# Performance work log

Measured on AMD Instinct MI355X. Metric: run time of the kernel, lower is better.

## Reference

```python
import jax, jax.numpy as jnp
import numpy as np


def setup_inputs() -> dict:
    key = jax.random.key(0)
    ks = jax.random.split(key, 8)
    B, N, D, E, S = 8, 4096, 1024, 64, 2
    H = D
    T = E * S  # total slots = 128
    return {
        "x": jax.random.normal(ks[0], (B, N, D), jnp.float32),
        "phi_w": jax.random.normal(ks[1], (T, D), jnp.float32) * 0.02,
        "fc1_w": jax.random.normal(ks[2], (E, H, D), jnp.float32) * 0.02,
        "fc1_b": jax.random.normal(ks[3], (E, H), jnp.float32) * 0.02,
        "fc2_w": jax.random.normal(ks[4], (E, D, H), jnp.float32) * 0.02,
        "fc2_b": jax.random.normal(ks[5], (E, D), jnp.float32) * 0.02,
        "out_w": jax.random.normal(ks[6], (D, D), jnp.float32) * 0.02,
        "out_b": jax.random.normal(ks[7], (D,), jnp.float32) * 0.02,
    }


def reference(x, phi_w, fc1_w, fc1_b, fc2_w, fc2_b, out_w, out_b):
    B, N, D = x.shape
    E, H, _ = fc1_w.shape
    T = phi_w.shape[0]
    S = T // E
    # dispatch logits: (B, N, T)
    logits = jnp.einsum('bnd,td->bnt', x, phi_w)
    dispatch_w = jax.nn.softmax(logits, axis=1)  # softmax over tokens
    combine_w = jax.nn.softmax(logits, axis=2)   # softmax over slots
    # dispatch: compress tokens -> slots, (B, T, D) -> (B, E, S, D)
    slots = jnp.einsum('bnt,bnd->btd', dispatch_w, x).reshape(B, E, S, D)
    # per-expert tiny MLP (no weight duplication over B)
    h = jnp.einsum('besd,ehd->besh', slots, fc1_w) + fc1_b[None, :, None, :]
    h = jax.nn.gelu(h, approximate=True)  # tanh approximation, matches torch
    out = jnp.einsum('besh,edh->besd', h, fc2_w) + fc2_b[None, :, None, :]
    out = out.reshape(B, T, D)
    # combine: expand slots -> tokens
    combined = jnp.einsum('bnt,btd->bnd', combine_w, out)
    output = jnp.einsum('bnd,od->bno', combined, out_w) + out_b
    aux_loss = jnp.asarray(0.0, dtype=x.dtype)
    return output, aux_loss
```

## Files before the change

### kernel.cpp

```cpp
#include <hip/hip_runtime.h>
#include <math.h>

#define B_ 8
#define N_ 4096
#define D_ 1024
#define E_ 64
#define T_ 128

using bf16   = __bf16;
using bf16x4 = __attribute__((ext_vector_type(4))) __bf16;
using bf16x8 = __attribute__((ext_vector_type(8))) __bf16;
using f32x4  = __attribute__((ext_vector_type(4))) float;

#define MFMA16(a, b, c) __builtin_amdgcn_mfma_f32_16x16x32_bf16(a, b, c, 0, 0, 0)
#define LDK 72

__device__ __forceinline__ bf16x8 ldsfrag(const bf16* p) {
  const int lane = threadIdx.x & 63;
  return *(const bf16x8*)(p + (lane & 15) * LDK + (lane >> 4) * 8);
}

__global__ void k_convert(const float* __restrict__ phi, const float* __restrict__ ow,
                          bf16* __restrict__ phi_bf, bf16* __restrict__ ow_bf)
{
  if (blockIdx.x < 128) {
    int i = blockIdx.x * 256 + threadIdx.x;
    float4 v = ((const float4*)phi)[i];
    ((bf16x4*)phi_bf)[i] = (bf16x4){(bf16)v.x, (bf16)v.y, (bf16)v.z, (bf16)v.w};
  } else {
    int i = (blockIdx.x - 128) * 256 + threadIdx.x;
    float4 v = ((const float4*)ow)[i];
    ((bf16x4*)ow_bf)[i] = (bf16x4){(bf16)v.x, (bf16)v.y, (bf16)v.z, (bf16)v.w};
  }
}

__global__ __launch_bounds__(256) void k_logits(
    const float* __restrict__ X, const bf16* __restrict__ Phi,
    float* __restrict__ L, bf16* __restrict__ Xbf)
{
  __shared__ bf16 As[64][LDK];
  __shared__ bf16 Bs[128][LDK];
  const int m0 = blockIdx.x * 64;
  const int tid = threadIdx.x;
  const int wave = tid >> 6, lane = tid & 63;
  const int wm = (wave >> 1) * 32;
  const int wn = (wave & 1) * 64;

  f32x4 acc[2][4];
#pragma unroll
  for (int i = 0; i < 2; ++i)
#pragma unroll
    for (int j = 0; j < 4; ++j) acc[i][j] = (f32x4){0.f, 0.f, 0.f, 0.f};

  const int ar = tid >> 2, ac = (tid & 3) * 16;
  const int br = tid >> 1, bc = (tid & 1) * 32;

  for (int k0 = 0; k0 < 1024; k0 += 64) {
    const float* xp = X + (long)(m0 + ar) * 1024 + k0 + ac;
    float4 v0 = *(const float4*)(xp + 0);
    float4 v1 = *(const float4*)(xp + 4);
    float4 v2 = *(const float4*)(xp + 8);
    float4 v3 = *(const float4*)(xp + 12);
    bf16x8 p0 = {(bf16)v0.x, (bf16)v0.y, (bf16)v0.z, (bf16)v0.w,
                 (bf16)v1.x, (bf16)v1.y, (bf16)v1.z, (bf16)v1.w};
    bf16x8 p1 = {(bf16)v2.x, (bf16)v2.y, (bf16)v2.z, (bf16)v2.w,
                 (bf16)v3.x, (bf16)v3.y, (bf16)v3.z, (bf16)v3.w};
    *(bf16x8*)&As[ar][ac]     = p0;
    *(bf16x8*)&As[ar][ac + 8] = p1;
    bf16* xo = Xbf + (long)(m0 + ar) * 1024 + k0 + ac;
    *(bf16x8*)xo       = p0;
    *(bf16x8*)(xo + 8) = p1;

    const bf16* pp = Phi + (long)br * 1024 + k0 + bc;
    *(bf16x8*)&Bs[br][bc + 0]  = *(const bf16x8*)(pp + 0);
    *(bf16x8*)&Bs[br][bc + 8]  = *(const bf16x8*)(pp + 8);
    *(bf16x8*)&Bs[br][bc + 16] = *(const bf16x8*)(pp + 16);
    *(bf16x8*)&Bs[br][bc + 24] = *(const bf16x8*)(pp + 24);
    __syncthreads();
#pragma unroll
    for (int kk = 0; kk < 64; kk += 32) {
      bf16x8 a0 = ldsfrag(&As[wm][kk]);
      bf16x8 a1 = ldsfrag(&As[wm + 16][kk]);
#pragma unroll
      for (int n = 0; n < 4; ++n) {
        bf16x8 bb = ldsfrag(&Bs[wn + n * 16][kk]);
        acc[0][n] = MFMA16(a0, bb, acc[0][n]);
        acc[1][n] = MFMA16(a1, bb, acc[1][n]);
      }
    }
    __syncthreads();
  }
  const int cc = lane & 15, rr = (lane >> 4) * 4;
#pragma unroll
  for (int m = 0; m < 2; ++m)
#pragma unroll
    for (int n = 0; n < 4; ++n)
#pragma unroll
      for (int j = 0; j < 4; ++j)
        L[(long)(m0 + wm + m * 16 + rr + j) * 128 + wn + n * 16 + cc] = acc[m][n][j];
}

__global__ __launch_bounds__(256) void disp_partial(const float* __restrict__ L,
    float* __restrict__ redM, float* __restrict__ redS)
{
  const int chunk = blockIdx.x;
  const int b     = blockIdx.y;
  const int t    = threadIdx.x & 127;
  const int half = threadIdx.x >> 7;
  const float* Lb = L + (long)b * N_ * T_;
  float m = -1e30f, s = 0.f;
  for (int i = 0; i < 64; ++i) {
    int n = chunk * 128 + i * 2 + half;
    float v = Lb[(long)n * T_ + t];
    if (v > m) { s = s * expf(m - v) + 1.f; m = v; }
    else       { s += expf(v - m); }
  }
  __shared__ float sm[128], ss[128];
  if (half) { sm[t] = m; ss[t] = s; }
  __syncthreads();
  if (!half) {
    float m2 = sm[t], s2 = ss[t];
    float nm = fmaxf(m, m2);
    float ns = s * expf(m - nm) + s2 * expf(m2 - nm);
    redM[((long)b * 32 + chunk) * 128 + t] = nm;
    redS[((long)b * 32 + chunk) * 128 + t] = ns;
  }
}

__global__ void disp_final(const float* __restrict__ redM, const float* __restrict__ redS,
                           float* __restrict__ Mf, float* __restrict__ Zf)
{
  int idx = blockIdx.x * 256 + threadIdx.x;
  int b = idx >> 7, t = idx & 127;
  float m = -1e30f, s = 0.f;
  for (int c = 0; c < 32; ++c) {
    float mc = redM[((long)b * 32 + c) * 128 + t];
    float sc = redS[((long)b * 32 + c) * 128 + t];
    float nm = fmaxf(m, mc);
    s = s * expf(m - nm) + sc * expf(mc - nm);
    m = nm;
  }
  Mf[idx] = m;
  Zf[idx] = 1.f / s;
}

__global__ __launch_bounds__(256) void k_dwt(const float* __restrict__ L,
    const float* __restrict__ Mf, const float* __restrict__ Zf, bf16* __restrict__ DWT)
{
  __shared__ float S[64][132];
  const int b = blockIdx.y, n0 = blockIdx.x * 64;
  const int tid = threadIdx.x;
  const int r = tid >> 2;
  const int c0 = (tid & 3) * 32;
  const float* Lp = L + ((long)b * N_ + n0 + r) * T_ + c0;
#pragma unroll
  for (int i = 0; i < 32; i += 4) {
    float4 v = *(const float4*)(Lp + i);
    int tb = b * 128 + c0 + i;
    S[r][c0 + i + 0] = expf(v.x - Mf[tb + 0]) * Zf[tb + 0];
    S[r][c0 + i + 1] = expf(v.y - Mf[tb + 1]) * Zf[tb + 1];
    S[r][c0 + i + 2] = expf(v.z - Mf[tb + 2]) * Zf[tb + 2];
    S[r][c0 + i + 3] = expf(v.w - Mf[tb + 3]) * Zf[tb + 3];
  }
  __syncthreads();
  const int nc = (tid & 7) * 8;
  for (int ti = tid >> 3; ti < 128; ti += 32) {
    bf16x8 o;
#pragma unroll
    for (int j = 0; j < 8; ++j) o[j] = (bf16)S[nc + j][ti];
    *(bf16x8*)(DWT + ((long)b * 128 + ti) * 4096 + n0 + nc) = o;
  }
}

__global__ __launch_bounds__(256) void k_cw(const float* __restrict__ L, bf16* __restrict__ CW)
{
  const int row  = blockIdx.x * 4 + (threadIdx.x >> 6);
  const int lane = threadIdx.x & 63;
  const float* Lr = L + (long)row * T_;
  float v0 = Lr[lane], v1 = Lr[lane + 64];
  float m = fmaxf(v0, v1);
#pragma unroll
  for (int o = 32; o; o >>= 1) m = fmaxf(m, __shfl_xor(m, o));
  float e0 = expf(v0 - m), e1 = expf(v1 - m);
  float s = e0 + e1;
#pragma unroll
  for (int o = 32; o; o >>= 1) s += __shfl_xor(s, o);
  float inv = 1.f / s;
  CW[(long)row * T_ + lane]      = (bf16)(e0 * inv);
  CW[(long)row * T_ + lane + 64] = (bf16)(e1 * inv);
}

__global__ __launch_bounds__(256) void k_slots(
    const bf16* __restrict__ DWT, const bf16* __restrict__ Xbf, float* __restrict__ Part)
{
  __shared__ bf16 As[128][LDK];
  __shared__ bf16 Bs[128][LDK];
  const int b = blockIdx.z >> 3, chunk = blockIdx.z & 7;
  const int d0 = blockIdx.x * 128;
  const int tid = threadIdx.x, wave = tid >> 6, lane = tid & 63;
  const int wm = (wave >> 1) * 64, wn = (wave & 1) * 64;

  f32x4 acc[4][4];
#pragma unroll
  for (int i = 0; i < 4; ++i)
#pragma unroll
    for (int j = 0; j < 4; ++j) acc[i][j] = (f32x4){0.f, 0.f, 0.f, 0.f};

  const int at = tid >> 1, anc = (tid & 1) * 32;
  const int bn = tid >> 2, bdc = (tid & 3) * 32;
  const long dwt_b = (long)b * 128 * 4096;
  const long x_b   = (long)b * 4096 * 1024;

  for (int k0 = 0; k0 < 512; k0 += 64) {
    const int nbase = chunk * 512 + k0;
    const bf16* ap = DWT + dwt_b + (long)at * 4096 + nbase + anc;
    *(bf16x8*)&As[at][anc + 0]  = *(const bf16x8*)(ap + 0);
    *(bf16x8*)&As[at][anc + 8]  = *(const bf16x8*)(ap + 8);
    *(bf16x8*)&As[at][anc + 16] = *(const bf16x8*)(ap + 16);
    *(bf16x8*)&As[at][anc + 24] = *(const bf16x8*)(ap + 24);
    const bf16* xp = Xbf + x_b + (long)(nbase + bn) * 1024 + d0 + bdc;
    bf16x8 q0 = *(const bf16x8*)(xp + 0);
    bf16x8 q1 = *(const bf16x8*)(xp + 8);
    bf16x8 q2 = *(const bf16x8*)(xp + 16);
    bf16x8 q3 = *(const bf16x8*)(xp + 24);
#pragma unroll
    for (int i = 0; i < 8; ++i) {
      Bs[bdc + i][bn]      = q0[i];
      Bs[bdc + 8 + i][bn]  = q1[i];
      Bs[bdc + 16 + i][bn] = q2[i];
      Bs[bdc + 24 + i][bn] = q3[i];
    }
    __syncthreads();
#pragma unroll
    for (int kk = 0; kk < 64; kk += 32) {
      bf16x8 af[4], bfr[4];
#pragma unroll
      for (int m = 0; m < 4; ++m) af[m]  = ldsfrag(&As[wm + m * 16][kk]);
#pragma unroll
      for (int n = 0; n < 4; ++n) bfr[n] = ldsfrag(&Bs[wn + n * 16][kk]);
#pragma unroll
      for (int m = 0; m < 4; ++m)
#pragma unroll
        for (int n = 0; n < 4; ++n)
          acc[m][n] = MFMA16(af[m], bfr[n], acc[m][n]);
    }
    __syncthreads();
  }
  const int cc = lane & 15, rr = (lane >> 4) * 4;
  float* Cp = Part + (long)(chunk * 8 + b) * 128 * 1024;
#pragma unroll
  for (int m = 0; m < 4; ++m)
#pragma unroll
    for (int n = 0; n < 4; ++n)
#pragma unroll
      for (int j = 0; j < 4; ++j)
        Cp[(long)(wm + m * 16 + rr + j) * 1024 + d0 + wn + n * 16 + cc] = acc[m][n][j];
}

__global__ void k_reduce8(const float* __restrict__ P, bf16* __restrict__ O)
{
  long base = ((long)blockIdx.x * 256 + threadIdx.x) * 4;
  float4 s = *(const float4*)(P + base);
  for (int c = 1; c < 8; ++c) {
    float4 v = *(const float4*)(P + (long)c * 1048576 + base);
    s.x += v.x; s.y += v.y; s.z += v.z; s.w += v.w;
  }
  *(bf16x4*)(O + base) = (bf16x4){(bf16)s.x, (bf16)s.y, (bf16)s.z, (bf16)s.w};
}

template<int GELU, int INL>
__global__ __launch_bounds__(256) void k_expert(
    const bf16* __restrict__ Ab, const float* __restrict__ W,
    const float* __restrict__ bias, bf16* __restrict__ Out)
{
  __shared__ bf16 As[16][LDK];
  __shared__ bf16 Bs[64][LDK];
  const int e = blockIdx.y;
  const int h0 = blockIdx.x * 64;
  const int tid = threadIdx.x, wave = tid >> 6, lane = tid & 63;
  f32x4 acc = (f32x4){0.f, 0.f, 0.f, 0.f};

  const int hr = tid >> 2, kc = (tid & 3) * 16;

  for (int k0 = 0; k0 < 1024; k0 += 64) {
    if (tid < 128) {
      int r = tid >> 3, akc = (tid & 7) * 8;
      long row = (INL == 0) ? (long)((r >> 1) * 128 + e * 2 + (r & 1)) : (long)(e * 16 + r);
      *(bf16x8*)&As[r][akc] = *(const bf16x8*)(Ab + row * 1024 + k0 + akc);
    }
    const float* wp = W + ((long)e * 1024 + h0 + hr) * 1024 + k0 + kc;
    float4 w0 = *(const float4*)(wp + 0);
    float4 w1 = *(const float4*)(wp + 4);
    float4 w2 = *(const float4*)(wp + 8);
    float4 w3 = *(const float4*)(wp + 12);
    bf16x8 p0 = {(bf16)w0.x, (bf16)w0.y, (bf16)w0.z, (bf16)w0.w,
                 (bf16)w1.x, (bf16)w1.y, (bf16)w1.z, (bf16)w1.w};
    bf16x8 p1 = {(bf16)w2.x, (bf16)w2.y, (bf16)w2.z, (bf16)w2.w,
                 (bf16)w3.x, (bf16)w3.y, (bf16)w3.z, (bf16)w3.w};
    *(bf16x8*)&Bs[hr][kc]     = p0;
    *(bf16x8*)&Bs[hr][kc + 8] = p1;
    __syncthreads();
#pragma unroll
    for (int kk = 0; kk < 64; kk += 32) {
      bf16x8 a  = ldsfrag(&As[0][kk]);
      bf16x8 bb = ldsfrag(&Bs[wave * 16][kk]);
      acc = MFMA16(a, bb, acc);
    }
    __syncthreads();
  }
  const int cc = lane & 15, rr = (lane >> 4) * 4;
  const int h = h0 + wave * 16 + cc;
  const float bs = bias[e * 1024 + h];
#pragma unroll
  for (int j = 0; j < 4; ++j) {
    float v = acc[j] + bs;
    if (GELU) {
      float x3 = v * v * v;
      v = 0.5f * v * (1.f + tanhf(0.7978845608028654f * (v + 0.044715f * x3)));
    }
    int m = rr + j;
    long orow = (INL == 0) ? (long)(e * 16 + m) : (long)((m >> 1) * 128 + e * 2 + (m & 1));
    Out[orow * 1024 + h] = (bf16)v;
  }
}

__global__ __launch_bounds__(256) void k_proj(
    const bf16* __restrict__ OWbf, const bf16* __restrict__ OS, bf16* __restrict__ PT)
{
  __shared__ bf16 As[64][LDK];
  __shared__ bf16 Bs[64][LDK];
  const int o0 = blockIdx.y * 64, t0 = blockIdx.x * 64;
  const int tid = threadIdx.x, wave = tid >> 6, lane = tid & 63;
  const int wm = (wave >> 1) * 32, wn = (wave & 1) * 32;
  f32x4 acc[2][2];
#pragma unroll
  for (int i = 0; i < 2; ++i)
#pragma unroll
    for (int j = 0; j < 2; ++j) acc[i][j] = (f32x4){0.f, 0.f, 0.f, 0.f};

  const int r = tid >> 2, kc = (tid & 3) * 16;
  for (int k0 = 0; k0 < 1024; k0 += 64) {
    const bf16* apo = OWbf + (long)(o0 + r) * 1024 + k0 + kc;
    *(bf16x8*)&As[r][kc]     = *(const bf16x8*)(apo + 0);
    *(bf16x8*)&As[r][kc + 8] = *(const bf16x8*)(apo + 8);
    const bf16* bpo = OS + (long)(t0 + r) * 1024 + k0 + kc;
    *(bf16x8*)&Bs[r][kc]     = *(const bf16x8*)(bpo + 0);
    *(bf16x8*)&Bs[r][kc + 8] = *(const bf16x8*)(bpo + 8);
    __syncthreads();
#pragma unroll
    for (int kk = 0; kk < 64; kk += 32) {
      bf16x8 a0 = ldsfrag(&As[wm][kk]);
      bf16x8 a1 = ldsfrag(&As[wm + 16][kk]);
      bf16x8 b0 = ldsfrag(&Bs[wn][kk]);
      bf16x8 b1 = ldsfrag(&Bs[wn + 16][kk]);
      acc[0][0] = MFMA16(a0, b0, acc[0][0]);
      acc[0][1] = MFMA16(a0, b1, acc[0][1]);
      acc[1][0] = MFMA16(a1, b0, acc[1][0]);
      acc[1][1] = MFMA16(a1, b1, acc[1][1]);
    }
    __syncthreads();
  }
  const int cc = lane & 15, rr = (lane >> 4) * 4;
#pragma unroll
  for (int m = 0; m < 2; ++m)
#pragma unroll
    for (int n = 0; n < 2; ++n)
#pragma unroll
      for (int j = 0; j < 4; ++j)
        PT[(long)(o0 + wm + m * 16 + rr + j) * 1024 + t0 + wn + n * 16 + cc] =
            (bf16)acc[m][n][j];
}

__global__ __launch_bounds__(256) void k_combine(
    const bf16* __restrict__ CW, const bf16* __restrict__ PT,
    const float* __restrict__ ob, float* __restrict__ O)
{
  __shared__ bf16 As[128][LDK];
  __shared__ bf16 Bs[128][LDK];
  const int b = blockIdx.z, m0 = blockIdx.y * 128, o0 = blockIdx.x * 128;
  const int tid = threadIdx.x, wave = tid >> 6, lane = tid & 63;
  const int wm = (wave >> 1) * 64, wn = (wave & 1) * 64;

  f32x4 acc[4][4];
#pragma unroll
  for (int i = 0; i < 4; ++i)
#pragma unroll
    for (int j = 0; j < 4; ++j) acc[i][j] = (f32x4){0.f, 0.f, 0.f, 0.f};

  const int r = tid >> 1, tc = (tid & 1) * 32;
  for (int k0 = 0; k0 < 128; k0 += 64) {
    const bf16* ap = CW + ((long)b * N_ + m0 + r) * 128 + k0 + tc;
    *(bf16x8*)&As[r][tc + 0]  = *(const bf16x8*)(ap + 0);
    *(bf16x8*)&As[r][tc + 8]  = *(const bf16x8*)(ap + 8);
    *(bf16x8*)&As[r][tc + 16] = *(const bf16x8*)(ap + 16);
    *(bf16x8*)&As[r][tc + 24] = *(const bf16x8*)(ap + 24);
    const bf16* bp = PT + (long)(o0 + r) * 1024 + b * 128 + k0 + tc;
    *(bf16x8*)&Bs[r][tc + 0]  = *(const bf16x8*)(bp + 0);
    *(bf16x8*)&Bs[r][tc + 8]  = *(const bf16x8*)(bp + 8);
    *(bf16x8*)&Bs[r][tc + 16] = *(const bf16x8*)(bp + 16);
    *(bf16x8*)&Bs[r][tc + 24] = *(const bf16x8*)(bp + 24);
    __syncthreads();
#pragma unroll
    for (int kk = 0; kk < 64; kk += 32) {
      bf16x8 af[4], bfr[4];
#pragma unroll
      for (int m = 0; m < 4; ++m) af[m]  = ldsfrag(&As[wm + m * 16][kk]);
#pragma unroll
      for (int n = 0; n < 4; ++n) bfr[n] = ldsfrag(&Bs[wn + n * 16][kk]);
#pragma unroll
      for (int m = 0; m < 4; ++m)
#pragma unroll
        for (int n = 0; n < 4; ++n)
          acc[m][n] = MFMA16(af[m], bfr[n], acc[m][n]);
    }
    __syncthreads();
  }
  const int cc = lane & 15, rr = (lane >> 4) * 4;
#pragma unroll
  for (int n = 0; n < 4; ++n) {
    const int o = o0 + wn + n * 16 + cc;
    const float bv = ob[o];
#pragma unroll
    for (int m = 0; m < 4; ++m)
#pragma unroll
      for (int j = 0; j < 4; ++j)
        O[((long)b * N_ + m0 + wm + m * 16 + rr + j) * 1024 + o] = acc[m][n][j] + bv;
  }
}

__global__ void write_aux(float* __restrict__ out) { out[(long)B_ * N_ * D_] = 0.f; }

extern "C" void kernel_launch(void* const* d_in, const int* in_sizes, int n_in,
                              void* d_out, int out_size, void* d_ws, size_t ws_size,
                              hipStream_t stream)
{
  const float* x     = (const float*)d_in[0];
  const float* phi_w = (const float*)d_in[1];
  const float* fc1_w = (const float*)d_in[2];
  const float* fc1_b = (const float*)d_in[3];
  const float* fc2_w = (const float*)d_in[4];
  const float* fc2_b = (const float*)d_in[5];
  const float* out_w = (const float*)d_in[6];
  const float* out_b = (const float*)d_in[7];
  float* out = (float*)d_out;

  float* ws     = (float*)d_ws;
  float* logits = ws;
  float* redM   = logits + 4194304;
  float* redS   = redM + 32768;
  float* Mf     = redS + 32768;
  float* Zf     = Mf + 1024;
  bf16* DWT     = (bf16*)(Zf + 1024);
  bf16* CW      = DWT + 4194304;
  bf16* slots   = CW + 4194304;
  bf16* hbuf    = slots + 1048576;
  bf16* outs    = hbuf + 1048576;
  bf16* projT   = outs + 1048576;
  bf16* phi_bf  = projT + 1048576;
  bf16* outw_bf = phi_bf + 131072;

  bf16* Xbf   = (bf16*)d_out;
  float* Part = (float*)d_out + 16777216;

  k_convert<<<dim3(1152), 256, 0, stream>>>(phi_w, out_w, phi_bf, outw_bf);
  k_logits<<<dim3(512), 256, 0, stream>>>(x, phi_bf, logits, Xbf);
  disp_partial<<<dim3(32, 8), 256, 0, stream>>>(logits, redM, redS);
  disp_final<<<dim3(4), 256, 0, stream>>>(redM, redS, Mf, Zf);
  k_dwt<<<dim3(64, 8), 256, 0, stream>>>(logits, Mf, Zf, DWT);
  k_cw<<<dim3(8192), 256, 0, stream>>>(logits, CW);
  k_slots<<<dim3(8, 1, 64), 256, 0, stream>>>(DWT, Xbf, Part);
  k_reduce8<<<dim3(1024), 256, 0, stream>>>(Part, slots);
  k_expert<1, 0><<<dim3(16, 64), 256, 0, stream>>>(slots, fc1_w, fc1_b, hbuf);
  k_expert<0, 1><<<dim3(16, 64), 256, 0, stream>>>(hbuf, fc2_w, fc2_b, outs);
  k_proj<<<dim3(16, 16), 256, 0, stream>>>(outw_bf, outs, projT);
  k_combine<<<dim3(8, 32, 8), 256, 0, stream>>>(CW, projT, out_b, out);
  write_aux<<<1, 1, 0, stream>>>(out);
}
```

Measured before the change: 344.1 us.

## Drop bf16 staging copies, fuse dispatch/combine weights, swizzle slots LDS, prefetch expert loads

Removes the separate weight-conversion kernel and the bf16 copy of x, so each GEMM converts fp32 to bf16 while loading tiles. The dispatch and combine softmax kernels are merged into one pass over the logits. k_slots reads fp32 x directly, writes its transposed tile with an XOR-swizzled LDS layout to cut bank conflicts, and uses 4 larger K chunks instead of 8, which shrinks the partial-sum reduction. The expert kernel register-prefetches the next tile. k_slots now reads twice the bytes of x (fp32 instead of bf16) and has fewer blocks, a possible cost.

New measurement: 364.1 us. +5.8%, slower.

```diff
diff --git a/kernel.cpp b/kernel.cpp
--- a/kernel.cpp
+++ b/kernel.cpp
@@ -20,23 +20,13 @@
   return *(const bf16x8*)(p + (lane & 15) * LDK + (lane >> 4) * 8);
 }
 
-__global__ void k_convert(const float* __restrict__ phi, const float* __restrict__ ow,
-                          bf16* __restrict__ phi_bf, bf16* __restrict__ ow_bf)
-{
-  if (blockIdx.x < 128) {
-    int i = blockIdx.x * 256 + threadIdx.x;
-    float4 v = ((const float4*)phi)[i];
-    ((bf16x4*)phi_bf)[i] = (bf16x4){(bf16)v.x, (bf16)v.y, (bf16)v.z, (bf16)v.w};
-  } else {
-    int i = (blockIdx.x - 128) * 256 + threadIdx.x;
-    float4 v = ((const float4*)ow)[i];
-    ((bf16x4*)ow_bf)[i] = (bf16x4){(bf16)v.x, (bf16)v.y, (bf16)v.z, (bf16)v.w};
-  }
+__device__ __forceinline__ bf16x8 cvt8(float4 a, float4 b) {
+  return (bf16x8){(bf16)a.x, (bf16)a.y, (bf16)a.z, (bf16)a.w,
+                  (bf16)b.x, (bf16)b.y, (bf16)b.z, (bf16)b.w};
 }
 
 __global__ __launch_bounds__(256) void k_logits(
-    const float* __restrict__ X, const bf16* __restrict__ Phi,
-    float* __restrict__ L, bf16* __restrict__ Xbf)
+    const float* __restrict__ X, const float* __restrict__ Phi, float* __restrict__ L)
 {
   __shared__ bf16 As[64][LDK];
   __shared__ bf16 Bs[128][LDK];
@@ -61,21 +51,22 @@
     float4 v1 = *(const float4*)(xp + 4);
     float4 v2 = *(const float4*)(xp + 8);
     float4 v3 = *(const float4*)(xp + 12);
-    bf16x8 p0 = {(bf16)v0.x, (bf16)v0.y, (bf16)v0.z, (bf16)v0.w,
-                 (bf16)v1.x, (bf16)v1.y, (bf16)v1.z, (bf16)v1.w};
-    bf16x8 p1 = {(bf16)v2.x, (bf16)v2.y, (bf16)v2.z, (bf16)v2.w,
-                 (bf16)v3.x, (bf16)v3.y, (bf16)v3.z, (bf16)v3.w};
-    *(bf16x8*)&As[ar][ac]     = p0;
-    *(bf16x8*)&As[ar][ac + 8] = p1;
-    bf16* xo = Xbf + (long)(m0 + ar) * 1024 + k0 + ac;
-    *(bf16x8*)xo       = p0;
-    *(bf16x8*)(xo + 8) = p1;
-
-    const bf16* pp = Phi + (long)br * 1024 + k0 + bc;
-    *(bf16x8*)&Bs[br][bc + 0]  = *(const bf16x8*)(pp + 0);
-    *(bf16x8*)&Bs[br][bc + 8]  = *(const bf16x8*)(pp + 8);
-    *(bf16x8*)&Bs[br][bc + 16] = *(const bf16x8*)(pp + 16);
-    *(bf16x8*)&Bs[br][bc + 24] = *(const bf16x8*)(pp + 24);
+    *(bf16x8*)&As[ar][ac]     = cvt8(v0, v1);
+    *(bf16x8*)&As[ar][ac + 8] = cvt8(v2, v3);
+
+    const float* pp = Phi + (long)br * 1024 + k0 + bc;
+    float4 p0 = *(const float4*)(pp + 0);
+    float4 p1 = *(const float4*)(pp + 4);
+    float4 p2 = *(const float4*)(pp + 8);
+    float4 p3 = *(const float4*)(pp + 12);
+    float4 p4 = *(const float4*)(pp + 16);
+    float4 p5 = *(const float4*)(pp + 20);
+    float4 p6 = *(const float4*)(pp + 24);
+    float4 p7 = *(const float4*)(pp + 28);
+    *(bf16x8*)&Bs[br][bc + 0]  = cvt8(p0, p1);
+    *(bf16x8*)&Bs[br][bc + 8]  = cvt8(p2, p3);
+    *(bf16x8*)&Bs[br][bc + 16] = cvt8(p4, p5);
+    *(bf16x8*)&Bs[br][bc + 24] = cvt8(p6, p7);
     __syncthreads();
 #pragma unroll
     for (int kk = 0; kk < 64; kk += 32) {
@@ -144,59 +135,67 @@
   Zf[idx] = 1.f / s;
 }
 
-__global__ __launch_bounds__(256) void k_dwt(const float* __restrict__ L,
-    const float* __restrict__ Mf, const float* __restrict__ Zf, bf16* __restrict__ DWT)
-{
-  __shared__ float S[64][132];
+__global__ __launch_bounds__(256) void k_weights(const float* __restrict__ L,
+    const float* __restrict__ Mf, const float* __restrict__ Zf,
+    bf16* __restrict__ DWT, bf16* __restrict__ CW)
+{
+  __shared__ float S[64][133];
   const int b = blockIdx.y, n0 = blockIdx.x * 64;
   const int tid = threadIdx.x;
-  const int r = tid >> 2;
-  const int c0 = (tid & 3) * 32;
-  const float* Lp = L + ((long)b * N_ + n0 + r) * T_ + c0;
-#pragma unroll
-  for (int i = 0; i < 32; i += 4) {
-    float4 v = *(const float4*)(Lp + i);
-    int tb = b * 128 + c0 + i;
-    S[r][c0 + i + 0] = expf(v.x - Mf[tb + 0]) * Zf[tb + 0];
-    S[r][c0 + i + 1] = expf(v.y - Mf[tb + 1]) * Zf[tb + 1];
-    S[r][c0 + i + 2] = expf(v.z - Mf[tb + 2]) * Zf[tb + 2];
-    S[r][c0 + i + 3] = expf(v.w - Mf[tb + 3]) * Zf[tb + 3];
-  }
+  const int r = tid >> 2, q = tid & 3;
+  const float* Lp = L + ((long)b * N_ + n0 + r) * T_;
+  float v[32];
+#pragma unroll
+  for (int i = 0; i < 8; ++i) {
+    float4 t4 = *(const float4*)(Lp + q * 4 + i * 16);
+    v[i*4+0] = t4.x; v[i*4+1] = t4.y; v[i*4+2] = t4.z; v[i*4+3] = t4.w;
+    S[r][q*4 + i*16 + 0] = t4.x;
+    S[r][q*4 + i*16 + 1] = t4.y;
+    S[r][q*4 + i*16 + 2] = t4.z;
+    S[r][q*4 + i*16 + 3] = t4.w;
+  }
+  float m = -1e30f;
+#pragma unroll
+  for (int i = 0; i < 32; ++i) m = fmaxf(m, v[i]);
+  m = fmaxf(m, __shfl_xor(m, 1));
+  m = fmaxf(m, __shfl_xor(m, 2));
+  float s = 0.f;
+#pragma unroll
+  for (int i = 0; i < 32; ++i) { v[i] = expf(v[i] - m); s += v[i]; }
+  s += __shfl_xor(s, 1);
+  s += __shfl_xor(s, 2);
+  const float inv = 1.f / s;
+  bf16* cwr = CW + ((long)b * N_ + n0 + r) * 128 + q * 4;
+#pragma unroll
+  for (int i = 0; i < 8; ++i)
+    *(bf16x4*)(cwr + i * 16) = (bf16x4){(bf16)(v[i*4+0]*inv), (bf16)(v[i*4+1]*inv),
+                                        (bf16)(v[i*4+2]*inv), (bf16)(v[i*4+3]*inv)};
   __syncthreads();
   const int nc = (tid & 7) * 8;
   for (int ti = tid >> 3; ti < 128; ti += 32) {
+    const float mf = Mf[b * 128 + ti], zf = Zf[b * 128 + ti];
     bf16x8 o;
 #pragma unroll
-    for (int j = 0; j < 8; ++j) o[j] = (bf16)S[nc + j][ti];
+    for (int j = 0; j < 8; ++j) o[j] = (bf16)(expf(S[nc + j][ti] - mf) * zf);
     *(bf16x8*)(DWT + ((long)b * 128 + ti) * 4096 + n0 + nc) = o;
   }
 }
 
-__global__ __launch_bounds__(256) void k_cw(const float* __restrict__ L, bf16* __restrict__ CW)
-{
-  const int row  = blockIdx.x * 4 + (threadIdx.x >> 6);
-  const int lane = threadIdx.x & 63;
-  const float* Lr = L + (long)row * T_;
-  float v0 = Lr[lane], v1 = Lr[lane + 64];
-  float m = fmaxf(v0, v1);
-#pragma unroll
-  for (int o = 32; o; o >>= 1) m = fmaxf(m, __shfl_xor(m, o));
-  float e0 = expf(v0 - m), e1 = expf(v1 - m);
-  float s = e0 + e1;
-#pragma unroll
-  for (int o = 32; o; o >>= 1) s += __shfl_xor(s, o);
-  float inv = 1.f / s;
-  CW[(long)row * T_ + lane]      = (bf16)(e0 * inv);
-  CW[(long)row * T_ + lane + 64] = (bf16)(e1 * inv);
+__device__ __forceinline__ bf16x8 ldsfragB(const bf16 (*Bs)[LDK], int dbase, int kk) {
+  const int l = threadIdx.x & 63;
+  const int d = dbase + (l & 15);
+  const int c = ((l >> 4) * 8 + kk) ^ (((d >> 5) & 3) << 3);
+  return *(const bf16x8*)(&Bs[d][c]);
 }
 
 __global__ __launch_bounds__(256) void k_slots(
-    const bf16* __restrict__ DWT, const bf16* __restrict__ Xbf, float* __restrict__ Part)
+    const bf16* __restrict__ DWT, const float* __restrict__ X, float* __restrict__ Part)
 {
   __shared__ bf16 As[128][LDK];
   __shared__ bf16 Bs[128][LDK];
-  const int b = blockIdx.z >> 3, chunk = blockIdx.z & 7;
   const int d0 = blockIdx.x * 128;
+  const int chunk = blockIdx.y;
+  const int b = blockIdx.z;
   const int tid = threadIdx.x, wave = tid >> 6, lane = tid & 63;
   const int wm = (wave >> 1) * 64, wn = (wave & 1) * 64;
 
@@ -207,29 +206,34 @@
     for (int j = 0; j < 4; ++j) acc[i][j] = (f32x4){0.f, 0.f, 0.f, 0.f};
 
   const int at = tid >> 1, anc = (tid & 1) * 32;
-  const int bn = tid >> 2, bdc = (tid & 3) * 32;
+  const int bn = tid >> 2, bq = tid & 3, bdc = bq * 32;
+  const int bcol = bn ^ (bq << 3);
   const long dwt_b = (long)b * 128 * 4096;
   const long x_b   = (long)b * 4096 * 1024;
 
-  for (int k0 = 0; k0 < 512; k0 += 64) {
-    const int nbase = chunk * 512 + k0;
+  for (int k0 = 0; k0 < 1024; k0 += 64) {
+    const int nbase = chunk * 1024 + k0;
     const bf16* ap = DWT + dwt_b + (long)at * 4096 + nbase + anc;
     *(bf16x8*)&As[at][anc + 0]  = *(const bf16x8*)(ap + 0);
     *(bf16x8*)&As[at][anc + 8]  = *(const bf16x8*)(ap + 8);
     *(bf16x8*)&As[at][anc + 16] = *(const bf16x8*)(ap + 16);
     *(bf16x8*)&As[at][anc + 24] = *(const bf16x8*)(ap + 24);
-    const bf16* xp = Xbf + x_b + (long)(nbase + bn) * 1024 + d0 + bdc;
-    bf16x8 q0 = *(const bf16x8*)(xp + 0);
-    bf16x8 q1 = *(const bf16x8*)(xp + 8);
-    bf16x8 q2 = *(const bf16x8*)(xp + 16);
-    bf16x8 q3 = *(const bf16x8*)(xp + 24);
-#pragma unroll
-    for (int i = 0; i < 8; ++i) {
-      Bs[bdc + i][bn]      = q0[i];
-      Bs[bdc + 8 + i][bn]  = q1[i];
-      Bs[bdc + 16 + i][bn] = q2[i];
-      Bs[bdc + 24 + i][bn] = q3[i];
-    }
+    const float* xp = X + x_b + (long)(nbase + bn) * 1024 + d0 + bdc;
+    float4 f0 = *(const float4*)(xp + 0);
+    float4 f1 = *(const float4*)(xp + 4);
+    float4 f2 = *(const float4*)(xp + 8);
+    float4 f3 = *(const float4*)(xp + 12);
+    float4 f4 = *(const float4*)(xp + 16);
+    float4 f5 = *(const float4*)(xp + 20);
+    float4 f6 = *(const float4*)(xp + 24);
+    float4 f7 = *(const float4*)(xp + 28);
+    float fv[32];
+    *(float4*)&fv[0]  = f0; *(float4*)&fv[4]  = f1;
+    *(float4*)&fv[8]  = f2; *(float4*)&fv[12] = f3;
+    *(float4*)&fv[16] = f4; *(float4*)&fv[20] = f5;
+    *(float4*)&fv[24] = f6; *(float4*)&fv[28] = f7;
+#pragma unroll
+    for (int i = 0; i < 32; ++i) Bs[bdc + i][bcol] = (bf16)fv[i];
     __syncthreads();
 #pragma unroll
     for (int kk = 0; kk < 64; kk += 32) {
@@ -237,7 +241,7 @@
 #pragma unroll
       for (int m = 0; m < 4; ++m) af[m]  = ldsfrag(&As[wm + m * 16][kk]);
 #pragma unroll
-      for (int n = 0; n < 4; ++n) bfr[n] = ldsfrag(&Bs[wn + n * 16][kk]);
+      for (int n = 0; n < 4; ++n) bfr[n] = ldsfragB(Bs, wn + n * 16, kk);
 #pragma unroll
       for (int m = 0; m < 4; ++m)
 #pragma unroll
@@ -247,7 +251,7 @@
     __syncthreads();
   }
   const int cc = lane & 15, rr = (lane >> 4) * 4;
-  float* Cp = Part + (long)(chunk * 8 + b) * 128 * 1024;
+  float* Cp = Part + ((long)chunk * 8 + b) * 128 * 1024;
 #pragma unroll
   for (int m = 0; m < 4; ++m)
 #pragma unroll
@@ -257,11 +261,11 @@
         Cp[(long)(wm + m * 16 + rr + j) * 1024 + d0 + wn + n * 16 + cc] = acc[m][n][j];
 }
 
-__global__ void k_reduce8(const float* __restrict__ P, bf16* __restrict__ O)
+__global__ void k_reduce4(const float* __restrict__ P, bf16* __restrict__ O)
 {
   long base = ((long)blockIdx.x * 256 + threadIdx.x) * 4;
   float4 s = *(const float4*)(P + base);
-  for (int c = 1; c < 8; ++c) {
+  for (int c = 1; c < 4; ++c) {
     float4 v = *(const float4*)(P + (long)c * 1048576 + base);
     s.x += v.x; s.y += v.y; s.z += v.z; s.w += v.w;
   }
@@ -281,31 +285,37 @@
   f32x4 acc = (f32x4){0.f, 0.f, 0.f, 0.f};
 
   const int hr = tid >> 2, kc = (tid & 3) * 16;
+  const float* wbase = W + ((long)e * 1024 + h0 + hr) * 1024 + kc;
+  const int ar = tid >> 3, akc = (tid & 7) * 8;
+  const long arow = (INL == 0) ? (long)((ar >> 1) * 128 + e * 2 + (ar & 1))
+                               : (long)(e * 16 + ar);
+  const bf16* abase = Ab + arow * 1024 + akc;
+
+  bf16x8 areg;
+  if (tid < 128) areg = *(const bf16x8*)(abase);
+  float4 w0 = *(const float4*)(wbase + 0);
+  float4 w1 = *(const float4*)(wbase + 4);
+  float4 w2 = *(const float4*)(wbase + 8);
+  float4 w3 = *(const float4*)(wbase + 12);
 
   for (int k0 = 0; k0 < 1024; k0 += 64) {
-    if (tid < 128) {
-      int r = tid >> 3, akc = (tid & 7) * 8;
-      long row = (INL == 0) ? (long)((r >> 1) * 128 + e * 2 + (r & 1)) : (long)(e * 16 + r);
-      *(bf16x8*)&As[r][akc] = *(const bf16x8*)(Ab + row * 1024 + k0 + akc);
-    }
-    const float* wp = W + ((long)e * 1024 + h0 + hr) * 1024 + k0 + kc;
-    float4 w0 = *(const float4*)(wp + 0);
-    float4 w1 = *(const float4*)(wp + 4);
-    float4 w2 = *(const float4*)(wp + 8);
-    float4 w3 = *(const float4*)(wp + 12);
-    bf16x8 p0 = {(bf16)w0.x, (bf16)w0.y, (bf16)w0.z, (bf16)w0.w,
-                 (bf16)w1.x, (bf16)w1.y, (bf16)w1.z, (bf16)w1.w};
-    bf16x8 p1 = {(bf16)w2.x, (bf16)w2.y, (bf16)w2.z, (bf16)w2.w,
-                 (bf16)w3.x, (bf16)w3.y, (bf16)w3.z, (bf16)w3.w};
-    *(bf16x8*)&Bs[hr][kc]     = p0;
-    *(bf16x8*)&Bs[hr][kc + 8] = p1;
-    __syncthreads();
-#pragma unroll
-    for (int kk = 0; kk < 64; kk += 32) {
-      bf16x8 a  = ldsfrag(&As[0][kk]);
-      bf16x8 bb = ldsfrag(&Bs[wave * 16][kk]);
-      acc = MFMA16(a, bb, acc);
-    }
+    if (tid < 128) *(bf16x8*)&As[ar][akc] = areg;
+    *(bf16x8*)&Bs[hr][kc]     = cvt8(w0, w1);
+    *(bf16x8*)&Bs[hr][kc + 8] = cvt8(w2, w3);
+    if (k0 < 960) {
+      if (tid < 128) areg = *(const bf16x8*)(abase + k0 + 64);
+      w0 = *(const float4*)(wbase + k0 + 64 + 0);
+      w1 = *(const float4*)(wbase + k0 + 64 + 4);
+      w2 = *(const float4*)(wbase + k0 + 64 + 8);
+      w3 = *(const float4*)(wbase + k0 + 64 + 12);
+    }
+    __syncthreads();
+    bf16x8 a0 = ldsfrag(&As[0][0]);
+    bf16x8 b0 = ldsfrag(&Bs[wave * 16][0]);
+    acc = MFMA16(a0, b0, acc);
+    a0 = ldsfrag(&As[0][32]);
+    b0 = ldsfrag(&Bs[wave * 16][32]);
+    acc = MFMA16(a0, b0, acc);
     __syncthreads();
   }
   const int cc = lane & 15, rr = (lane >> 4) * 4;
@@ -325,7 +335,7 @@
 }
 
 __global__ __launch_bounds__(256) void k_proj(
-    const bf16* __restrict__ OWbf, const bf16* __restrict__ OS, bf16* __restrict__ PT)
+    const float* __restrict__ OW, const bf16* __restrict__ OS, bf16* __restrict__ PT)
 {
   __shared__ bf16 As[64][LDK];
   __shared__ bf16 Bs[64][LDK];
@@ -340,23 +350,27 @@
 
   const int r = tid >> 2, kc = (tid & 3) * 16;
   for (int k0 = 0; k0 < 1024; k0 += 64) {
-    const bf16* apo = OWbf + (long)(o0 + r) * 1024 + k0 + kc;
-    *(bf16x8*)&As[r][kc]     = *(const bf16x8*)(apo + 0);
-    *(bf16x8*)&As[r][kc + 8] = *(const bf16x8*)(apo + 8);
+    const float* apo = OW + (long)(o0 + r) * 1024 + k0 + kc;
+    float4 a0 = *(const float4*)(apo + 0);
+    float4 a1 = *(const float4*)(apo + 4);
+    float4 a2 = *(const float4*)(apo + 8);
+    float4 a3 = *(const float4*)(apo + 12);
+    *(bf16x8*)&As[r][kc]     = cvt8(a0, a1);
+    *(bf16x8*)&As[r][kc + 8] = cvt8(a2, a3);
     const bf16* bpo = OS + (long)(t0 + r) * 1024 + k0 + kc;
     *(bf16x8*)&Bs[r][kc]     = *(const bf16x8*)(bpo + 0);
     *(bf16x8*)&Bs[r][kc + 8] = *(const bf16x8*)(bpo + 8);
     __syncthreads();
 #pragma unroll
     for (int kk = 0; kk < 64; kk += 32) {
-      bf16x8 a0 = ldsfrag(&As[wm][kk]);
-      bf16x8 a1 = ldsfrag(&As[wm + 16][kk]);
-      bf16x8 b0 = ldsfrag(&Bs[wn][kk]);
-      bf16x8 b1 = ldsfrag(&Bs[wn + 16][kk]);
-      acc[0][0] = MFMA16(a0, b0, acc[0][0]);
-      acc[0][1] = MFMA16(a0, b1, acc[0][1]);
-      acc[1][0] = MFMA16(a1, b0, acc[1][0]);
-      acc[1][1] = MFMA16(a1, b1, acc[1][1]);
+      bf16x8 a0f = ldsfrag(&As[wm][kk]);
+      bf16x8 a1f = ldsfrag(&As[wm + 16][kk]);
+      bf16x8 b0f = ldsfrag(&Bs[wn][kk]);
+      bf16x8 b1f = ldsfrag(&Bs[wn + 16][kk]);
+      acc[0][0] = MFMA16(a0f, b0f, acc[0][0]);
+      acc[0][1] = MFMA16(a0f, b1f, acc[0][1]);
+      acc[1][0] = MFMA16(a1f, b0f, acc[1][0]);
+      acc[1][1] = MFMA16(a1f, b1f, acc[1][1]);
     }
     __syncthreads();
   }
@@ -456,23 +470,17 @@
   bf16* hbuf    = slots + 1048576;
   bf16* outs    = hbuf + 1048576;
   bf16* projT   = outs + 1048576;
-  bf16* phi_bf  = projT + 1048576;
-  bf16* outw_bf = phi_bf + 131072;
-
-  bf16* Xbf   = (bf16*)d_out;
-  float* Part = (float*)d_out + 16777216;
-
-  k_convert<<<dim3(1152), 256, 0, stream>>>(phi_w, out_w, phi_bf, outw_bf);
-  k_logits<<<dim3(512), 256, 0, stream>>>(x, phi_bf, logits, Xbf);
+  float* Part   = (float*)(projT + 1048576);
+
+  k_logits<<<dim3(512), 256, 0, stream>>>(x, phi_w, logits);
   disp_partial<<<dim3(32, 8), 256, 0, stream>>>(logits, redM, redS);
   disp_final<<<dim3(4), 256, 0, stream>>>(redM, redS, Mf, Zf);
-  k_dwt<<<dim3(64, 8), 256, 0, stream>>>(logits, Mf, Zf, DWT);
-  k_cw<<<dim3(8192), 256, 0, stream>>>(logits, CW);
-  k_slots<<<dim3(8, 1, 64), 256, 0, stream>>>(DWT, Xbf, Part);
-  k_reduce8<<<dim3(1024), 256, 0, stream>>>(Part, slots);
+  k_weights<<<dim3(64, 8), 256, 0, stream>>>(logits, Mf, Zf, DWT, CW);
+  k_slots<<<dim3(8, 4, 8), 256, 0, stream>>>(DWT, x, Part);
+  k_reduce4<<<dim3(1024), 256, 0, stream>>>(Part, slots);
   k_expert<1, 0><<<dim3(16, 64), 256, 0, stream>>>(slots, fc1_w, fc1_b, hbuf);
   k_expert<0, 1><<<dim3(16, 64), 256, 0, stream>>>(hbuf, fc2_w, fc2_b, outs);
-  k_proj<<<dim3(16, 16), 256, 0, stream>>>(outw_bf, outs, projT);
+  k_proj<<<dim3(16, 16), 256, 0, stream>>>(out_w, outs, projT);
   k_combine<<<dim3(8, 32, 8), 256, 0, stream>>>(CW, projT, out_b, out);
   write_aux<<<1, 1, 0, stream>>>(out);
 }
```
